# Optimization experiments

Measured on AMD Instinct MI355X. Metric: run time of the kernel, lower is better.

Reference implementation:

```python
import jax, jax.numpy as jnp
import numpy as np


def _safe_pow(v, p):
    # mimic torch.nan_to_num(pow(v, p), nan=0, posinf=0, neginf=0) for v >= 0
    out = jnp.where(v > 0, jnp.power(jnp.where(v > 0, v, 1.0), p), 0.0)
    return out.astype(jnp.float32)


def setup_inputs() -> dict:
    key = jax.random.key(0)
    k1, k2, k3 = jax.random.split(key, 3)
    N, E, Din, Dout = 20000, 4096, 128, 128
    x = jax.random.normal(k1, (N, Din), dtype=jnp.float32)
    H = jax.random.uniform(k2, (N, E), dtype=jnp.float32)
    W = jax.random.normal(k3, (Dout, Din), dtype=jnp.float32) * (1.0 / np.sqrt(Din))
    b = jnp.zeros((Dout,), dtype=jnp.float32)
    return {"x": x, "H": H, "W": W, "b": b}


def reference(x, H, W, b):
    # Dv^{-1/2}: node degrees; De^{-1}: hyperedge degrees.
    # torch.diag(...)**p with nan/inf->0 is exactly diagonal scaling, so we
    # use broadcasted vector scaling fused around the two GEMMs.
    dv = _safe_pow(jnp.sum(H, axis=-1), -0.5)   # [N]
    de = _safe_pow(jnp.sum(H, axis=0), -1.0)    # [E]
    x = dv[:, None] * x                          # Dv^{-1/2} x
    x = H.T @ x                                  # [E, Din]
    x = de[:, None] * x                          # De^{-1}
    x = H @ x                                    # [N, Din]
    x = dv[:, None] * x                          # Dv^{-1/2}
    return x @ W.T + b                           # Linear
```

## Files before the change

### kernel.cpp

```cpp
#include <hip/hip_runtime.h>
#include <hip/hip_bf16.h>
#include <stdint.h>


#define N_ 20000
#define E_ 4096
#define D_ 128
#define NPAD 20032
#define XTB_S 20032

typedef __attribute__((ext_vector_type(8))) short    bf16x8;
typedef __attribute__((ext_vector_type(4))) float    f32x4;
typedef __attribute__((ext_vector_type(8))) unsigned short us8;
typedef __attribute__((ext_vector_type(4))) unsigned short us4;

__device__ __forceinline__ unsigned short f2bf(float f) {
  unsigned u = __float_as_uint(f);
  u += 0x7FFFu + ((u >> 16) & 1u);
  return (unsigned short)(u >> 16);
}
__device__ __forceinline__ unsigned cvtpk(float lo, float hi) {
  unsigned r;
  asm("v_cvt_pk_bf16_f32 %0, %1, %2" : "=v"(r) : "v"(lo), "v"(hi));
  return r;
}
__device__ __forceinline__ void gload16(const unsigned short* g, unsigned short* l) {
  __builtin_amdgcn_global_load_lds(
      (const __attribute__((address_space(1))) unsigned int*)g,
      (__attribute__((address_space(3))) unsigned int*)l, 16, 0, 0);
}

__global__ __launch_bounds__(256) void k_pre(const float* __restrict__ H,
                                             const float* __restrict__ x,
                                             float* __restrict__ dv,
                                             unsigned short* __restrict__ Hb,
                                             unsigned short* __restrict__ xTb) {
  const int t = threadIdx.x, lane = t & 63, w = t >> 6;
  const int b = blockIdx.x;
  if (b >= 2500) {
    const size_t base = (size_t)(20000 + (b - 2500) * 8) * E_;
    for (int i = t; i < 4096; i += 256)
      *(us8*)&Hb[base + (size_t)i * 8] = (us8){0,0,0,0,0,0,0,0};
    if (b == 2500 && t < 128) {
#pragma unroll
      for (int c = 0; c < 4; ++c)
        *(us8*)&xTb[(size_t)t * XTB_S + 20000 + c * 8] = (us8){0,0,0,0,0,0,0,0};
    }
    return;
  }
  __shared__ float red[32];
  __shared__ float xt[8 * 128];
  const int n0 = b * 8;
  { int r = t >> 5, d4 = (t & 31) * 4;
    *(f32x4*)&xt[r * 128 + d4] = *(const f32x4*)(x + (size_t)(n0 + r) * D_ + d4); }
  float rs[8];
#pragma unroll
  for (int r = 0; r < 8; ++r) {
    rs[r] = 0.f;
    const float* rp = H + (size_t)(n0 + r) * E_;
    unsigned short* hp = Hb + (size_t)(n0 + r) * E_;
#pragma unroll
    for (int j = 0; j < 4; ++j) {
      f32x4 v = *(const f32x4*)(rp + j * 1024 + t * 4);
      rs[r] += (v.x + v.y) + (v.z + v.w);
      union { us4 v4; unsigned u32[2]; } un;
      un.u32[0] = cvtpk(v.x, v.y);
      un.u32[1] = cvtpk(v.z, v.w);
      *(us4*)(hp + j * 1024 + t * 4) = un.v4;
    }
  }
#pragma unroll
  for (int r = 0; r < 8; ++r)
#pragma unroll
    for (int off = 32; off; off >>= 1) rs[r] += __shfl_xor(rs[r], off);
  if (lane == 0) {
#pragma unroll
    for (int r = 0; r < 8; ++r) red[w * 8 + r] = rs[r];
  }
  __syncthreads();
  if (t < 8) {
    float s = red[t] + red[8 + t] + red[16 + t] + red[24 + t];
    float d = s > 0.f ? rsqrtf(s) : 0.f;
    dv[n0 + t] = d;
    red[t] = d;
  }
  __syncthreads();
  if (t < 128) {
    int d = t;
    float v[8];
#pragma unroll
    for (int r = 0; r < 8; ++r) v[r] = xt[r * 128 + d] * red[r];
    union { us8 v8; unsigned u32[4]; } un;
#pragma unroll
    for (int j = 0; j < 4; ++j) un.u32[j] = cvtpk(v[2 * j], v[2 * j + 1]);
    *(us8*)(xTb + (size_t)d * XTB_S + n0) = un.v8;
  }
}

__global__ __launch_bounds__(256) void k_fin(const float* __restrict__ desum,
                                             float* __restrict__ de) {
  int e = blockIdx.x * 256 + threadIdx.x;
  float s = desum[e];
  de[e] = s > 0.f ? 1.f / s : 0.f;
}

__global__ __launch_bounds__(256) void k_wb(const float* __restrict__ W,
                                            unsigned short* __restrict__ Wb) {
  int tid = blockIdx.x * 256 + threadIdx.x;
  float4 v = *(const float4*)(W + (size_t)tid * 4);
  union { us4 v; unsigned short u[4]; } un;
  un.u[0] = f2bf(v.x); un.u[1] = f2bf(v.y); un.u[2] = f2bf(v.z); un.u[3] = f2bf(v.w);
  *(us4*)(Wb + (size_t)tid * 4) = un.v;
}

__global__ __launch_bounds__(256) void k_gemm1(const unsigned short* __restrict__ Hb,
                                               const unsigned short* __restrict__ xTb,
                                               float* __restrict__ partialT,
                                               float* __restrict__ desum) {
  __shared__ unsigned short lH[2][64 * 64];
  __shared__ unsigned short lX[2][128 * 64];
  const int t = threadIdx.x, lane = t & 63, w = t >> 6;
  const int eb = blockIdx.x & 63, s = blockIdx.x >> 6;
  const int e0 = eb * 64;
  const int nsteps = 39 + (s == 7);
  const int g0 = s * 39;
  const int lrow = lane >> 3, lslot = lane & 7;
  const int bswz = (lslot ^ lrow) << 3;
  const int wy = w >> 1, wx = w & 1;
  const int ep = t & 31, q = t >> 5;
  const int er0 = 2 * ep, er1 = 2 * ep + 1;
  const int sl0 = (q ^ (er0 & 7)) << 3, sl1 = (q ^ (er1 & 7)) << 3;

  f32x4 acc[4][2];
  f32x4 accC[2];
#pragma unroll
  for (int i = 0; i < 4; ++i)
#pragma unroll
    for (int j = 0; j < 2; ++j) acc[i][j] = (f32x4){0.f, 0.f, 0.f, 0.f};
  accC[0] = (f32x4){0.f, 0.f, 0.f, 0.f};
  accC[1] = (f32x4){0.f, 0.f, 0.f, 0.f};
  bf16x8 ones;
#pragma unroll
  for (int i = 0; i < 8; ++i) ones[i] = (short)0x3F80;

  unsigned hr[8];
  auto LOADH = [&](int g) {
    const unsigned short* p = Hb + (size_t)(g * 64 + q * 8) * E_ + e0 + er0;
#pragma unroll
    for (int j = 0; j < 8; ++j) hr[j] = *(const unsigned*)(p + (size_t)j * E_);
  };
  auto WRITEH = [&](int bufi) {
    union { bf16x8 v; unsigned u[4]; } lo, hi;
#pragma unroll
    for (int p = 0; p < 4; ++p) {
      lo.u[p] = (hr[2 * p] & 0xFFFFu) | (hr[2 * p + 1] << 16);
      hi.u[p] = (hr[2 * p] >> 16) | (hr[2 * p + 1] & 0xFFFF0000u);
    }
    *(bf16x8*)&lH[bufi][er0 * 64 + sl0] = lo.v;
    *(bf16x8*)&lH[bufi][er1 * 64 + sl1] = hi.v;
  };
  auto GLOADX = [&](int g, int bufi) {
#pragma unroll
    for (int i = 0; i < 4; ++i) {
      int c = w * 4 + i;
      gload16(xTb + (size_t)(8 * c + lrow) * XTB_S + g * 64 + bswz,
              &lX[bufi][c * 512]);
    }
  };

  LOADH(g0); GLOADX(g0, 0); WRITEH(0);
  __syncthreads();
  int cur = 0;
  for (int it = 0; it < nsteps; ++it) {
    bool hn = it + 1 < nsteps;
    if (hn) { LOADH(g0 + it + 1); GLOADX(g0 + it + 1, cur ^ 1); }
    const int kg = lane >> 4, fr = lane & 15;
    bf16x8 ax[4][2], bh[2][2];
#pragma unroll
    for (int mi = 0; mi < 4; ++mi) {
      int m = wy * 64 + mi * 16 + fr;
#pragma unroll
      for (int kk = 0; kk < 2; ++kk)
        ax[mi][kk] = *(const bf16x8*)&lX[cur][m * 64 + (((kk * 4 + kg) ^ (m & 7)) << 3)];
    }
#pragma unroll
    for (int ni = 0; ni < 2; ++ni) {
      int n = wx * 32 + ni * 16 + fr;
#pragma unroll
      for (int kk = 0; kk < 2; ++kk)
        bh[ni][kk] = *(const bf16x8*)&lH[cur][n * 64 + (((kk * 4 + kg) ^ (n & 7)) << 3)];
    }
#pragma unroll
    for (int kk = 0; kk < 2; ++kk)
#pragma unroll
      for (int mi = 0; mi < 4; ++mi)
#pragma unroll
        for (int ni = 0; ni < 2; ++ni)
          acc[mi][ni] = __builtin_amdgcn_mfma_f32_16x16x32_bf16(ax[mi][kk], bh[ni][kk], acc[mi][ni], 0, 0, 0);
    if (wy == 0) {
#pragma unroll
      for (int kk = 0; kk < 2; ++kk)
#pragma unroll
        for (int ni = 0; ni < 2; ++ni)
          accC[ni] = __builtin_amdgcn_mfma_f32_16x16x32_bf16(ones, bh[ni][kk], accC[ni], 0, 0, 0);
    }
    if (hn) WRITEH(cur ^ 1);
    __syncthreads();
    cur ^= 1;
  }
  const int kg = lane >> 4, fr = lane & 15;
  if (wy == 0 && kg == 0) {
#pragma unroll
    for (int ni = 0; ni < 2; ++ni)
      atomicAdd(&desum[e0 + wx * 32 + ni * 16 + fr], accC[ni][0]);
  }
#pragma unroll
  for (int mi = 0; mi < 4; ++mi)
#pragma unroll
    for (int ni = 0; ni < 2; ++ni)
#pragma unroll
      for (int r = 0; r < 4; ++r) {
        int d = wy * 64 + mi * 16 + kg * 4 + r;
        int e = e0 + wx * 32 + ni * 16 + fr;
        partialT[((size_t)s * 128 + d) * E_ + e] = acc[mi][ni][r];
      }
}

__global__ __launch_bounds__(256) void k_reduce1(const float* __restrict__ partialT,
                                                 const float* __restrict__ de,
                                                 unsigned short* __restrict__ x3T) {
  int tid = blockIdx.x * 256 + threadIdx.x;
  int d = tid >> 12, e = tid & 4095;
  float s = 0.f;
#pragma unroll
  for (int ss = 0; ss < 8; ++ss) s += partialT[((size_t)ss * 128 + d) * E_ + e];
  x3T[(size_t)d * E_ + e] = f2bf(de[e] * s);
}

__global__ __launch_bounds__(256) void k_gemm2(const unsigned short* __restrict__ Hb,
                                               const unsigned short* __restrict__ x3T,
                                               const unsigned short* __restrict__ Wb,
                                               const float* __restrict__ dv,
                                               const float* __restrict__ bias,
                                               float* __restrict__ out) {
  __shared__ unsigned short sm[2 * 64 * 64 + 2 * 128 * 64];
  __shared__ unsigned short lW[128 * 128];
  unsigned short (*lA)[64 * 64]  = (unsigned short (*)[64 * 64])sm;
  unsigned short (*lB)[128 * 64] = (unsigned short (*)[128 * 64])(sm + 2 * 64 * 64);
  unsigned short* lC = sm;
  const int t = threadIdx.x, lane = t & 63, w = t >> 6;
  const int n0b = blockIdx.x * 64;
  const int lrow = lane >> 3, lslot = lane & 7;
  const int bswz = (lslot ^ lrow) << 3;
  const int wy = w >> 1, wx = w & 1;

  {
    int j = t >> 1;
#pragma unroll
    for (int jj = 0; jj < 4; ++jj) {
      int dofs = (t & 1) * 64 + jj * 16;
      const us8* src = (const us8*)(Wb + (size_t)j * 128 + dofs);
      *(us8*)&lW[j * 128 + dofs]     = src[0];
      *(us8*)&lW[j * 128 + dofs + 8] = src[1];
    }
  }

  auto GLOADA = [&](int g, int bufi) {
#pragma unroll
    for (int i = 0; i < 2; ++i) {
      int c = w * 2 + i;
      gload16(Hb + (size_t)(n0b + 8 * c + lrow) * E_ + g * 64 + bswz,
              &lA[bufi][c * 512]);
    }
  };
  auto GLOADB = [&](int g, int bufi) {
#pragma unroll
    for (int i = 0; i < 4; ++i) {
      int c = w * 4 + i;
      gload16(x3T + (size_t)(8 * c + lrow) * E_ + g * 64 + bswz,
              &lB[bufi][c * 512]);
    }
  };

  f32x4 acc[2][4];
#pragma unroll
  for (int i = 0; i < 2; ++i)
#pragma unroll
    for (int j = 0; j < 4; ++j) acc[i][j] = (f32x4){0.f, 0.f, 0.f, 0.f};

  GLOADA(0, 0); GLOADB(0, 0);
  __syncthreads();
  int cur = 0;
  for (int it = 0; it < 64; ++it) {
    bool hn = it < 63;
    if (hn) { GLOADA(it + 1, cur ^ 1); GLOADB(it + 1, cur ^ 1); }
    const int kg = lane >> 4, fr = lane & 15;
    bf16x8 af[2][2], bfr[4][2];
#pragma unroll
    for (int mi = 0; mi < 2; ++mi) {
      int m = wy * 32 + mi * 16 + fr;
#pragma unroll
      for (int kk = 0; kk < 2; ++kk)
        af[mi][kk] = *(const bf16x8*)&lA[cur][m * 64 + (((kk * 4 + kg) ^ (m & 7)) << 3)];
    }
#pragma unroll
    for (int ni = 0; ni < 4; ++ni) {
      int d = wx * 64 + ni * 16 + fr;
#pragma unroll
      for (int kk = 0; kk < 2; ++kk)
        bfr[ni][kk] = *(const bf16x8*)&lB[cur][d * 64 + (((kk * 4 + kg) ^ (d & 7)) << 3)];
    }
#pragma unroll
    for (int kk = 0; kk < 2; ++kk)
#pragma unroll
      for (int mi = 0; mi < 2; ++mi)
#pragma unroll
        for (int ni = 0; ni < 4; ++ni)
          acc[mi][ni] = __builtin_amdgcn_mfma_f32_16x16x32_bf16(af[mi][kk], bfr[ni][kk], acc[mi][ni], 0, 0, 0);
    __syncthreads();
    cur ^= 1;
  }
#pragma unroll
  for (int mi = 0; mi < 2; ++mi) {
    float dvv[4];
#pragma unroll
    for (int r = 0; r < 4; ++r)
      dvv[r] = dv[min(n0b + wy * 32 + mi * 16 + (lane >> 4) * 4 + r, N_ - 1)];
#pragma unroll
    for (int ni = 0; ni < 4; ++ni)
#pragma unroll
      for (int r = 0; r < 4; ++r) {
        int row = wy * 32 + mi * 16 + (lane >> 4) * 4 + r;
        int col = wx * 64 + ni * 16 + (lane & 15);
        lC[row * 136 + col] = f2bf(acc[mi][ni][r] * dvv[r]);
      }
  }
  __syncthreads();
  f32x4 acc2[2][4];
#pragma unroll
  for (int i = 0; i < 2; ++i)
#pragma unroll
    for (int j = 0; j < 4; ++j) acc2[i][j] = (f32x4){0.f, 0.f, 0.f, 0.f};
#pragma unroll
  for (int ks = 0; ks < 4; ++ks) {
    int kofs = ks * 32 + (lane >> 4) * 8;
    bf16x8 a2[2], b2[4];
#pragma unroll
    for (int mi = 0; mi < 2; ++mi) {
      int m = wy * 32 + mi * 16 + (lane & 15);
      a2[mi] = *(const bf16x8*)&lC[m * 136 + kofs];
    }
#pragma unroll
    for (int ni = 0; ni < 4; ++ni) {
      int j = wx * 64 + ni * 16 + (lane & 15);
      b2[ni] = *(const bf16x8*)&lW[j * 128 + kofs];
    }
#pragma unroll
    for (int mi = 0; mi < 2; ++mi)
#pragma unroll
      for (int ni = 0; ni < 4; ++ni)
        acc2[mi][ni] = __builtin_amdgcn_mfma_f32_16x16x32_bf16(a2[mi], b2[ni], acc2[mi][ni], 0, 0, 0);
  }
#pragma unroll
  for (int mi = 0; mi < 2; ++mi)
#pragma unroll
    for (int ni = 0; ni < 4; ++ni) {
      int j = wx * 64 + ni * 16 + (lane & 15);
      float bb = bias[j];
#pragma unroll
      for (int r = 0; r < 4; ++r) {
        int n = n0b + wy * 32 + mi * 16 + (lane >> 4) * 4 + r;
        if (n < N_) out[(size_t)n * D_ + j] = acc2[mi][ni][r] + bb;
      }
    }
}

extern "C" void kernel_launch(void* const* d_in, const int* in_sizes, int n_in,
                              void* d_out, int out_size, void* d_ws, size_t ws_size,
                              hipStream_t stream) {
  const float* x = (const float*)d_in[0];
  const float* H = (const float*)d_in[1];
  const float* W = (const float*)d_in[2];
  const float* b = (const float*)d_in[3];
  float* out = (float*)d_out;
  char* ws = (char*)d_ws;
  float*          desum    = (float*)(ws);
  float*          de       = (float*)(ws + 16384);
  float*          dv       = (float*)(ws + 32768);
  unsigned short* Wb       = (unsigned short*)(ws + 112896);
  unsigned short* xTb      = (unsigned short*)(ws + 145664);
  unsigned short* x3T      = (unsigned short*)(ws + 5273856);
  float*          partialT = (float*)(ws + 6322432);
  unsigned short* Hb       = (unsigned short*)(ws + 23099648);

  hipMemsetAsync(desum, 0, 16384, stream);
  k_pre<<<2504, 256, 0, stream>>>(H, x, dv, Hb, xTb);
  k_wb<<<16, 256, 0, stream>>>(W, Wb);
  k_gemm1<<<512, 256, 0, stream>>>(Hb, xTb, partialT, desum);
  k_fin<<<16, 256, 0, stream>>>(desum, de);
  k_reduce1<<<2048, 256, 0, stream>>>(partialT, de, x3T);
  k_gemm2<<<313, 256, 0, stream>>>(Hb, x3T, Wb, dv, b, out);
}
```

Baseline: 240.7 us.

## Fold degree finalize and W conversion into neighbors; halve gemm2 row tile

Replaces the desum atomics and memset with per-split partial edge-degree stores, which k_reduce1 sums and inverts inline. k_reduce1 is vectorized to 8 elements per thread. The standalone W-to-bf16 kernel is removed and W is converted inside k_gemm2, which now uses 32-row tiles across 625 blocks for better CU coverage. This removes three launches and a memset, at the cost of redundant W conversion in every gemm2 block and less reuse of x3T per block.

```diff
diff --git a/kernel.cpp b/kernel.cpp
--- a/kernel.cpp
+++ b/kernel.cpp
@@ -6,7 +6,6 @@
 #define N_ 20000
 #define E_ 4096
 #define D_ 128
-#define NPAD 20032
 #define XTB_S 20032
 
 typedef __attribute__((ext_vector_type(8))) short    bf16x8;
@@ -97,26 +96,10 @@
   }
 }
 
-__global__ __launch_bounds__(256) void k_fin(const float* __restrict__ desum,
-                                             float* __restrict__ de) {
-  int e = blockIdx.x * 256 + threadIdx.x;
-  float s = desum[e];
-  de[e] = s > 0.f ? 1.f / s : 0.f;
-}
-
-__global__ __launch_bounds__(256) void k_wb(const float* __restrict__ W,
-                                            unsigned short* __restrict__ Wb) {
-  int tid = blockIdx.x * 256 + threadIdx.x;
-  float4 v = *(const float4*)(W + (size_t)tid * 4);
-  union { us4 v; unsigned short u[4]; } un;
-  un.u[0] = f2bf(v.x); un.u[1] = f2bf(v.y); un.u[2] = f2bf(v.z); un.u[3] = f2bf(v.w);
-  *(us4*)(Wb + (size_t)tid * 4) = un.v;
-}
-
 __global__ __launch_bounds__(256) void k_gemm1(const unsigned short* __restrict__ Hb,
                                                const unsigned short* __restrict__ xTb,
                                                float* __restrict__ partialT,
-                                               float* __restrict__ desum) {
+                                               float* __restrict__ desumP) {
   __shared__ unsigned short lH[2][64 * 64];
   __shared__ unsigned short lX[2][128 * 64];
   const int t = threadIdx.x, lane = t & 63, w = t >> 6;
@@ -212,7 +195,7 @@
   if (wy == 0 && kg == 0) {
 #pragma unroll
     for (int ni = 0; ni < 2; ++ni)
-      atomicAdd(&desum[e0 + wx * 32 + ni * 16 + fr], accC[ni][0]);
+      desumP[s * E_ + e0 + wx * 32 + ni * 16 + fr] = accC[ni][0];
   }
 #pragma unroll
   for (int mi = 0; mi < 4; ++mi)
@@ -227,51 +210,73 @@
 }
 
 __global__ __launch_bounds__(256) void k_reduce1(const float* __restrict__ partialT,
-                                                 const float* __restrict__ de,
+                                                 const float* __restrict__ desumP,
                                                  unsigned short* __restrict__ x3T) {
   int tid = blockIdx.x * 256 + threadIdx.x;
-  int d = tid >> 12, e = tid & 4095;
-  float s = 0.f;
-#pragma unroll
-  for (int ss = 0; ss < 8; ++ss) s += partialT[((size_t)ss * 128 + d) * E_ + e];
-  x3T[(size_t)d * E_ + e] = f2bf(de[e] * s);
+  int d = tid >> 9;
+  int e0 = (tid & 511) * 8;
+  f32x4 sA = {0.f,0.f,0.f,0.f}, sB = {0.f,0.f,0.f,0.f};
+  f32x4 dA = {0.f,0.f,0.f,0.f}, dB = {0.f,0.f,0.f,0.f};
+#pragma unroll
+  for (int ss = 0; ss < 8; ++ss) {
+    const float* p = partialT + ((size_t)ss * 128 + d) * E_ + e0;
+    sA += *(const f32x4*)p;
+    sB += *(const f32x4*)(p + 4);
+    const float* qd = desumP + ss * E_ + e0;
+    dA += *(const f32x4*)qd;
+    dB += *(const f32x4*)(qd + 4);
+  }
+  float sv[8] = {sA.x, sA.y, sA.z, sA.w, sB.x, sB.y, sB.z, sB.w};
+  float dvv[8] = {dA.x, dA.y, dA.z, dA.w, dB.x, dB.y, dB.z, dB.w};
+  float o[8];
+#pragma unroll
+  for (int i = 0; i < 8; ++i)
+    o[i] = dvv[i] > 0.f ? sv[i] / dvv[i] : 0.f;
+  union { us8 v8; unsigned u32[4]; } un;
+#pragma unroll
+  for (int j = 0; j < 4; ++j) un.u32[j] = cvtpk(o[2 * j], o[2 * j + 1]);
+  *(us8*)(x3T + (size_t)d * E_ + e0) = un.v8;
 }
 
 __global__ __launch_bounds__(256) void k_gemm2(const unsigned short* __restrict__ Hb,
                                                const unsigned short* __restrict__ x3T,
-                                               const unsigned short* __restrict__ Wb,
+                                               const float* __restrict__ W,
                                                const float* __restrict__ dv,
                                                const float* __restrict__ bias,
                                                float* __restrict__ out) {
-  __shared__ unsigned short sm[2 * 64 * 64 + 2 * 128 * 64];
-  __shared__ unsigned short lW[128 * 128];
-  unsigned short (*lA)[64 * 64]  = (unsigned short (*)[64 * 64])sm;
-  unsigned short (*lB)[128 * 64] = (unsigned short (*)[128 * 64])(sm + 2 * 64 * 64);
+  __shared__ unsigned short sm[2 * 32 * 64 + 2 * 128 * 64];
+  __shared__ unsigned short lW[128 * 136];
+  unsigned short (*lA)[32 * 64]  = (unsigned short (*)[32 * 64])sm;
+  unsigned short (*lB)[128 * 64] = (unsigned short (*)[128 * 64])(sm + 2 * 32 * 64);
   unsigned short* lC = sm;
   const int t = threadIdx.x, lane = t & 63, w = t >> 6;
-  const int n0b = blockIdx.x * 64;
+  const int n0b = blockIdx.x * 32;
   const int lrow = lane >> 3, lslot = lane & 7;
   const int bswz = (lslot ^ lrow) << 3;
   const int wy = w >> 1, wx = w & 1;
 
   {
     int j = t >> 1;
+    int dbase = (t & 1) * 64;
 #pragma unroll
     for (int jj = 0; jj < 4; ++jj) {
-      int dofs = (t & 1) * 64 + jj * 16;
-      const us8* src = (const us8*)(Wb + (size_t)j * 128 + dofs);
-      *(us8*)&lW[j * 128 + dofs]     = src[0];
-      *(us8*)&lW[j * 128 + dofs + 8] = src[1];
+      int dofs = dbase + jj * 16;
+      const float* wp = W + (size_t)j * 128 + dofs;
+      f32x4 a = *(const f32x4*)wp,       bq = *(const f32x4*)(wp + 4);
+      f32x4 c = *(const f32x4*)(wp + 8), dq = *(const f32x4*)(wp + 12);
+      union { us8 v; unsigned u[4]; } u0, u1;
+      u0.u[0] = cvtpk(a.x, a.y);  u0.u[1] = cvtpk(a.z, a.w);
+      u0.u[2] = cvtpk(bq.x, bq.y); u0.u[3] = cvtpk(bq.z, bq.w);
+      u1.u[0] = cvtpk(c.x, c.y);  u1.u[1] = cvtpk(c.z, c.w);
+      u1.u[2] = cvtpk(dq.x, dq.y); u1.u[3] = cvtpk(dq.z, dq.w);
+      *(us8*)&lW[j * 136 + dofs]     = u0.v;
+      *(us8*)&lW[j * 136 + dofs + 8] = u1.v;
     }
   }
 
   auto GLOADA = [&](int g, int bufi) {
-#pragma unroll
-    for (int i = 0; i < 2; ++i) {
-      int c = w * 2 + i;
-      gload16(Hb + (size_t)(n0b + 8 * c + lrow) * E_ + g * 64 + bswz,
-              &lA[bufi][c * 512]);
-    }
+    gload16(Hb + (size_t)(n0b + 8 * w + lrow) * E_ + g * 64 + bswz,
+            &lA[bufi][w * 512]);
   };
   auto GLOADB = [&](int g, int bufi) {
 #pragma unroll
@@ -282,11 +287,9 @@
     }
   };
 
-  f32x4 acc[2][4];
-#pragma unroll
-  for (int i = 0; i < 2; ++i)
-#pragma unroll
-    for (int j = 0; j < 4; ++j) acc[i][j] = (f32x4){0.f, 0.f, 0.f, 0.f};
+  f32x4 acc[4];
+#pragma unroll
+  for (int j = 0; j < 4; ++j) acc[j] = (f32x4){0.f, 0.f, 0.f, 0.f};
 
   GLOADA(0, 0); GLOADB(0, 0);
   __syncthreads();
@@ -295,14 +298,11 @@
     bool hn = it < 63;
     if (hn) { GLOADA(it + 1, cur ^ 1); GLOADB(it + 1, cur ^ 1); }
     const int kg = lane >> 4, fr = lane & 15;
-    bf16x8 af[2][2], bfr[4][2];
-#pragma unroll
-    for (int mi = 0; mi < 2; ++mi) {
-      int m = wy * 32 + mi * 16 + fr;
-#pragma unroll
-      for (int kk = 0; kk < 2; ++kk)
-        af[mi][kk] = *(const bf16x8*)&lA[cur][m * 64 + (((kk * 4 + kg) ^ (m & 7)) << 3)];
-    }
+    const int m = wy * 16 + fr;
+    bf16x8 af[2], bfr[4][2];
+#pragma unroll
+    for (int kk = 0; kk < 2; ++kk)
+      af[kk] = *(const bf16x8*)&lA[cur][m * 64 + (((kk * 4 + kg) ^ (m & 7)) << 3)];
 #pragma unroll
     for (int ni = 0; ni < 4; ++ni) {
       int d = wx * 64 + ni * 16 + fr;
@@ -313,66 +313,49 @@
 #pragma unroll
     for (int kk = 0; kk < 2; ++kk)
 #pragma unroll
-      for (int mi = 0; mi < 2; ++mi)
-#pragma unroll
-        for (int ni = 0; ni < 4; ++ni)
-          acc[mi][ni] = __builtin_amdgcn_mfma_f32_16x16x32_bf16(af[mi][kk], bfr[ni][kk], acc[mi][ni], 0, 0, 0);
+      for (int ni = 0; ni < 4; ++ni)
+        acc[ni] = __builtin_amdgcn_mfma_f32_16x16x32_bf16(af[kk], bfr[ni][kk], acc[ni], 0, 0, 0);
     __syncthreads();
     cur ^= 1;
   }
-#pragma unroll
-  for (int mi = 0; mi < 2; ++mi) {
-    float dvv[4];
-#pragma unroll
-    for (int r = 0; r < 4; ++r)
-      dvv[r] = dv[min(n0b + wy * 32 + mi * 16 + (lane >> 4) * 4 + r, N_ - 1)];
+  const int kg = lane >> 4, fr = lane & 15;
+  float dvv[4];
+#pragma unroll
+  for (int r = 0; r < 4; ++r) dvv[r] = dv[n0b + wy * 16 + kg * 4 + r];
+#pragma unroll
+  for (int ni = 0; ni < 4; ++ni)
+#pragma unroll
+    for (int r = 0; r < 4; ++r) {
+      int row = wy * 16 + kg * 4 + r;
+      int col = wx * 64 + ni * 16 + fr;
+      lC[row * 136 + col] = f2bf(acc[ni][r] * dvv[r]);
+    }
+  __syncthreads();
+  f32x4 acc2[4];
+#pragma unroll
+  for (int j = 0; j < 4; ++j) acc2[j] = (f32x4){0.f, 0.f, 0.f, 0.f};
+#pragma unroll
+  for (int ks = 0; ks < 4; ++ks) {
+    int kofs = ks * 32 + kg * 8;
+    bf16x8 a2 = *(const bf16x8*)&lC[(wy * 16 + fr) * 136 + kofs];
+    bf16x8 b2[4];
 #pragma unroll
     for (int ni = 0; ni < 4; ++ni)
-#pragma unroll
-      for (int r = 0; r < 4; ++r) {
-        int row = wy * 32 + mi * 16 + (lane >> 4) * 4 + r;
-        int col = wx * 64 + ni * 16 + (lane & 15);
-        lC[row * 136 + col] = f2bf(acc[mi][ni][r] * dvv[r]);
-      }
-  }
-  __syncthreads();
-  f32x4 acc2[2][4];
-#pragma unroll
-  for (int i = 0; i < 2; ++i)
-#pragma unroll
-    for (int j = 0; j < 4; ++j) acc2[i][j] = (f32x4){0.f, 0.f, 0.f, 0.f};
-#pragma unroll
-  for (int ks = 0; ks < 4; ++ks) {
-    int kofs = ks * 32 + (lane >> 4) * 8;
-    bf16x8 a2[2], b2[4];
-#pragma unroll
-    for (int mi = 0; mi < 2; ++mi) {
-      int m = wy * 32 + mi * 16 + (lane & 15);
-      a2[mi] = *(const bf16x8*)&lC[m * 136 + kofs];
-    }
-#pragma unroll
-    for (int ni = 0; ni < 4; ++ni) {
-      int j = wx * 64 + ni * 16 + (lane & 15);
-      b2[ni] = *(const bf16x8*)&lW[j * 128 + kofs];
-    }
-#pragma unroll
-    for (int mi = 0; mi < 2; ++mi)
-#pragma unroll
-      for (int ni = 0; ni < 4; ++ni)
-        acc2[mi][ni] = __builtin_amdgcn_mfma_f32_16x16x32_bf16(a2[mi], b2[ni], acc2[mi][ni], 0, 0, 0);
-  }
-#pragma unroll
-  for (int mi = 0; mi < 2; ++mi)
-#pragma unroll
-    for (int ni = 0; ni < 4; ++ni) {
-      int j = wx * 64 + ni * 16 + (lane & 15);
-      float bb = bias[j];
-#pragma unroll
-      for (int r = 0; r < 4; ++r) {
-        int n = n0b + wy * 32 + mi * 16 + (lane >> 4) * 4 + r;
-        if (n < N_) out[(size_t)n * D_ + j] = acc2[mi][ni][r] + bb;
-      }
-    }
+      b2[ni] = *(const bf16x8*)&lW[(wx * 64 + ni * 16 + fr) * 136 + kofs];
+#pragma unroll
+    for (int ni = 0; ni < 4; ++ni)
+      acc2[ni] = __builtin_amdgcn_mfma_f32_16x16x32_bf16(a2, b2[ni], acc2[ni], 0, 0, 0);
+  }
+#pragma unroll
+  for (int ni = 0; ni < 4; ++ni) {
+    int j = wx * 64 + ni * 16 + fr;
+    float bb = bias[j];
+#pragma unroll
+    for (int r = 0; r < 4; ++r) {
+      int n = n0b + wy * 16 + kg * 4 + r;
+      out[(size_t)n * D_ + j] = acc2[ni][r] + bb;
+    }
+  }
 }
 
 extern "C" void kernel_launch(void* const* d_in, const int* in_sizes, int n_in,
@@ -384,20 +367,15 @@
   const float* b = (const float*)d_in[3];
   float* out = (float*)d_out;
   char* ws = (char*)d_ws;
-  float*          desum    = (float*)(ws);
-  float*          de       = (float*)(ws + 16384);
-  float*          dv       = (float*)(ws + 32768);
-  unsigned short* Wb       = (unsigned short*)(ws + 112896);
-  unsigned short* xTb      = (unsigned short*)(ws + 145664);
-  unsigned short* x3T      = (unsigned short*)(ws + 5273856);
-  float*          partialT = (float*)(ws + 6322432);
-  unsigned short* Hb       = (unsigned short*)(ws + 23099648);
-
-  hipMemsetAsync(desum, 0, 16384, stream);
+  float*          desumP   = (float*)(ws);
+  float*          dv       = (float*)(ws + 131072);
+  unsigned short* xTb      = (unsigned short*)(ws + 211200);
+  unsigned short* x3T      = (unsigned short*)(ws + 5339392);
+  float*          partialT = (float*)(ws + 6387968);
+  unsigned short* Hb       = (unsigned short*)(ws + 23165184);
+
   k_pre<<<2504, 256, 0, stream>>>(H, x, dv, Hb, xTb);
-  k_wb<<<16, 256, 0, stream>>>(W, Wb);
-  k_gemm1<<<512, 256, 0, stream>>>(Hb, xTb, partialT, desum);
-  k_fin<<<16, 256, 0, stream>>>(desum, de);
-  k_reduce1<<<2048, 256, 0, stream>>>(partialT, de, x3T);
-  k_gemm2<<<313, 256, 0, stream>>>(Hb, x3T, Wb, dv, b, out);
-}
+  k_gemm1<<<512, 256, 0, stream>>>(Hb, xTb, partialT, desumP);
+  k_reduce1<<<256, 256, 0, stream>>>(partialT, desumP, x3T);
+  k_gemm2<<<625, 256, 0, stream>>>(Hb, x3T, W, dv, b, out);
+}
```

New measurement: 269.0 us. 1.12x slower.

## Widen GEMM1 edge tiles, split K sixteen ways, fuse degree finalize and W conversion

Applied to the files above, without the earlier changes.

GEMM1 now uses 128-wide hyperedge tiles and a 16-way split of the node dimension, so more work shares each x tile load. Per-split edge-degree partials replace the atomics and memset, and the reduce kernel sums them with vectorized loads, doing the reciprocal scaling in place. The separate k_fin and k_wb launches are removed, and W is converted to bf16 inside GEMM2 with a swizzled LDS layout. The price is twice the partialT traffic written and reduced, a larger LDS footprint, and more accumulator registers under launch_bounds(256,2).

```diff
diff --git a/kernel.cpp b/kernel.cpp
--- a/kernel.cpp
+++ b/kernel.cpp
@@ -6,8 +6,8 @@
 #define N_ 20000
 #define E_ 4096
 #define D_ 128
-#define NPAD 20032
 #define XTB_S 20032
+#define SPLIT 16
 
 typedef __attribute__((ext_vector_type(8))) short    bf16x8;
 typedef __attribute__((ext_vector_type(4))) float    f32x4;
@@ -97,67 +97,56 @@
   }
 }
 
-__global__ __launch_bounds__(256) void k_fin(const float* __restrict__ desum,
-                                             float* __restrict__ de) {
-  int e = blockIdx.x * 256 + threadIdx.x;
-  float s = desum[e];
-  de[e] = s > 0.f ? 1.f / s : 0.f;
-}
-
-__global__ __launch_bounds__(256) void k_wb(const float* __restrict__ W,
-                                            unsigned short* __restrict__ Wb) {
-  int tid = blockIdx.x * 256 + threadIdx.x;
-  float4 v = *(const float4*)(W + (size_t)tid * 4);
-  union { us4 v; unsigned short u[4]; } un;
-  un.u[0] = f2bf(v.x); un.u[1] = f2bf(v.y); un.u[2] = f2bf(v.z); un.u[3] = f2bf(v.w);
-  *(us4*)(Wb + (size_t)tid * 4) = un.v;
-}
-
-__global__ __launch_bounds__(256) void k_gemm1(const unsigned short* __restrict__ Hb,
-                                               const unsigned short* __restrict__ xTb,
-                                               float* __restrict__ partialT,
-                                               float* __restrict__ desum) {
-  __shared__ unsigned short lH[2][64 * 64];
+__global__ __launch_bounds__(256, 2) void k_gemm1(const unsigned short* __restrict__ Hb,
+                                                  const unsigned short* __restrict__ xTb,
+                                                  float* __restrict__ partialT,
+                                                  float* __restrict__ desumP) {
+  __shared__ unsigned short lH[2][128 * 68];
   __shared__ unsigned short lX[2][128 * 64];
   const int t = threadIdx.x, lane = t & 63, w = t >> 6;
-  const int eb = blockIdx.x & 63, s = blockIdx.x >> 6;
-  const int e0 = eb * 64;
-  const int nsteps = 39 + (s == 7);
-  const int g0 = s * 39;
+  const int bid = blockIdx.x;
+  const int j0 = bid >> 3;
+  const int s  = (bid & 7) * 2 + (j0 >> 5);
+  const int eb = j0 & 31;
+  const int e0 = eb * 128;
+  const int g0 = (s * 313) >> 4;
+  const int g1 = ((s + 1) * 313) >> 4;
   const int lrow = lane >> 3, lslot = lane & 7;
   const int bswz = (lslot ^ lrow) << 3;
   const int wy = w >> 1, wx = w & 1;
-  const int ep = t & 31, q = t >> 5;
-  const int er0 = 2 * ep, er1 = 2 * ep + 1;
-  const int sl0 = (q ^ (er0 & 7)) << 3, sl1 = (q ^ (er1 & 7)) << 3;
-
-  f32x4 acc[4][2];
+
+  f32x4 acc[4][4];
   f32x4 accC[2];
 #pragma unroll
   for (int i = 0; i < 4; ++i)
 #pragma unroll
-    for (int j = 0; j < 2; ++j) acc[i][j] = (f32x4){0.f, 0.f, 0.f, 0.f};
+    for (int j = 0; j < 4; ++j) acc[i][j] = (f32x4){0.f, 0.f, 0.f, 0.f};
   accC[0] = (f32x4){0.f, 0.f, 0.f, 0.f};
   accC[1] = (f32x4){0.f, 0.f, 0.f, 0.f};
   bf16x8 ones;
 #pragma unroll
   for (int i = 0; i < 8; ++i) ones[i] = (short)0x3F80;
 
-  unsigned hr[8];
+  unsigned hr[16];
   auto LOADH = [&](int g) {
-    const unsigned short* p = Hb + (size_t)(g * 64 + q * 8) * E_ + e0 + er0;
-#pragma unroll
-    for (int j = 0; j < 8; ++j) hr[j] = *(const unsigned*)(p + (size_t)j * E_);
+    const unsigned short* p = Hb + (size_t)(g * 64 + w * 16) * E_ + e0 + 2 * lane;
+#pragma unroll
+    for (int j = 0; j < 16; ++j)
+      hr[j] = *(const unsigned*)(p + (size_t)j * E_);
   };
   auto WRITEH = [&](int bufi) {
-    union { bf16x8 v; unsigned u[4]; } lo, hi;
-#pragma unroll
-    for (int p = 0; p < 4; ++p) {
-      lo.u[p] = (hr[2 * p] & 0xFFFFu) | (hr[2 * p + 1] << 16);
-      hi.u[p] = (hr[2 * p] >> 16) | (hr[2 * p + 1] & 0xFFFF0000u);
-    }
-    *(bf16x8*)&lH[bufi][er0 * 64 + sl0] = lo.v;
-    *(bf16x8*)&lH[bufi][er1 * 64 + sl1] = hi.v;
+#pragma unroll
+    for (int j = 0; j < 2; ++j) {
+      union { bf16x8 v; unsigned u[4]; } lo, hi;
+#pragma unroll
+      for (int p2 = 0; p2 < 4; ++p2) {
+        unsigned a = hr[j * 8 + 2 * p2], b = hr[j * 8 + 2 * p2 + 1];
+        lo.u[p2] = (a & 0xFFFFu) | (b << 16);
+        hi.u[p2] = (a >> 16) | (b & 0xFFFF0000u);
+      }
+      *(bf16x8*)&lH[bufi][(2 * lane) * 68 + (2 * w + j) * 8]     = lo.v;
+      *(bf16x8*)&lH[bufi][(2 * lane + 1) * 68 + (2 * w + j) * 8] = hi.v;
+    }
   };
   auto GLOADX = [&](int g, int bufi) {
 #pragma unroll
@@ -171,11 +160,11 @@
   LOADH(g0); GLOADX(g0, 0); WRITEH(0);
   __syncthreads();
   int cur = 0;
-  for (int it = 0; it < nsteps; ++it) {
-    bool hn = it + 1 < nsteps;
-    if (hn) { LOADH(g0 + it + 1); GLOADX(g0 + it + 1, cur ^ 1); }
+  for (int it = g0; it < g1; ++it) {
+    bool hn = it + 1 < g1;
+    if (hn) { LOADH(it + 1); GLOADX(it + 1, cur ^ 1); }
     const int kg = lane >> 4, fr = lane & 15;
-    bf16x8 ax[4][2], bh[2][2];
+    bf16x8 ax[4][2], bh[4][2];
 #pragma unroll
     for (int mi = 0; mi < 4; ++mi) {
       int m = wy * 64 + mi * 16 + fr;
@@ -184,62 +173,78 @@
         ax[mi][kk] = *(const bf16x8*)&lX[cur][m * 64 + (((kk * 4 + kg) ^ (m & 7)) << 3)];
     }
 #pragma unroll
-    for (int ni = 0; ni < 2; ++ni) {
-      int n = wx * 32 + ni * 16 + fr;
+    for (int ni = 0; ni < 4; ++ni) {
+      int n = wx * 64 + ni * 16 + fr;
 #pragma unroll
       for (int kk = 0; kk < 2; ++kk)
-        bh[ni][kk] = *(const bf16x8*)&lH[cur][n * 64 + (((kk * 4 + kg) ^ (n & 7)) << 3)];
+        bh[ni][kk] = *(const bf16x8*)&lH[cur][n * 68 + (kk * 4 + kg) * 8];
     }
 #pragma unroll
     for (int kk = 0; kk < 2; ++kk)
 #pragma unroll
       for (int mi = 0; mi < 4; ++mi)
 #pragma unroll
-        for (int ni = 0; ni < 2; ++ni)
+        for (int ni = 0; ni < 4; ++ni)
           acc[mi][ni] = __builtin_amdgcn_mfma_f32_16x16x32_bf16(ax[mi][kk], bh[ni][kk], acc[mi][ni], 0, 0, 0);
-    if (wy == 0) {
-#pragma unroll
-      for (int kk = 0; kk < 2; ++kk)
-#pragma unroll
-        for (int ni = 0; ni < 2; ++ni)
-          accC[ni] = __builtin_amdgcn_mfma_f32_16x16x32_bf16(ones, bh[ni][kk], accC[ni], 0, 0, 0);
-    }
+#pragma unroll
+    for (int kk = 0; kk < 2; ++kk)
+#pragma unroll
+      for (int ci = 0; ci < 2; ++ci)
+        accC[ci] = __builtin_amdgcn_mfma_f32_16x16x32_bf16(ones, bh[wy * 2 + ci][kk], accC[ci], 0, 0, 0);
     if (hn) WRITEH(cur ^ 1);
     __syncthreads();
     cur ^= 1;
   }
   const int kg = lane >> 4, fr = lane & 15;
-  if (wy == 0 && kg == 0) {
-#pragma unroll
-    for (int ni = 0; ni < 2; ++ni)
-      atomicAdd(&desum[e0 + wx * 32 + ni * 16 + fr], accC[ni][0]);
+  if (kg == 0) {
+#pragma unroll
+    for (int ci = 0; ci < 2; ++ci)
+      desumP[s * E_ + e0 + wx * 64 + (wy * 2 + ci) * 16 + fr] = accC[ci][0];
   }
 #pragma unroll
   for (int mi = 0; mi < 4; ++mi)
 #pragma unroll
-    for (int ni = 0; ni < 2; ++ni)
+    for (int ni = 0; ni < 4; ++ni)
 #pragma unroll
       for (int r = 0; r < 4; ++r) {
         int d = wy * 64 + mi * 16 + kg * 4 + r;
-        int e = e0 + wx * 32 + ni * 16 + fr;
+        int e = e0 + wx * 64 + ni * 16 + fr;
         partialT[((size_t)s * 128 + d) * E_ + e] = acc[mi][ni][r];
       }
 }
 
 __global__ __launch_bounds__(256) void k_reduce1(const float* __restrict__ partialT,
-                                                 const float* __restrict__ de,
+                                                 const float* __restrict__ desumP,
                                                  unsigned short* __restrict__ x3T) {
   int tid = blockIdx.x * 256 + threadIdx.x;
-  int d = tid >> 12, e = tid & 4095;
-  float s = 0.f;
-#pragma unroll
-  for (int ss = 0; ss < 8; ++ss) s += partialT[((size_t)ss * 128 + d) * E_ + e];
-  x3T[(size_t)d * E_ + e] = f2bf(de[e] * s);
+  int d = tid >> 9;
+  int e0 = (tid & 511) * 8;
+  f32x4 sA = {0.f,0.f,0.f,0.f}, sB = {0.f,0.f,0.f,0.f};
+  f32x4 dA = {0.f,0.f,0.f,0.f}, dB = {0.f,0.f,0.f,0.f};
+#pragma unroll
+  for (int ss = 0; ss < SPLIT; ++ss) {
+    const float* p = partialT + ((size_t)ss * 128 + d) * E_ + e0;
+    sA += *(const f32x4*)p;
+    sB += *(const f32x4*)(p + 4);
+    const float* qd = desumP + ss * E_ + e0;
+    dA += *(const f32x4*)qd;
+    dB += *(const f32x4*)(qd + 4);
+  }
+  float sv[8] = {sA.x, sA.y, sA.z, sA.w, sB.x, sB.y, sB.z, sB.w};
+  float dvv[8] = {dA.x, dA.y, dA.z, dA.w, dB.x, dB.y, dB.z, dB.w};
+  float o[8];
+#pragma unroll
+  for (int i = 0; i < 8; ++i)
+    o[i] = dvv[i] > 0.f ? sv[i] / dvv[i] : 0.f;
+  union { us8 v8; unsigned u32[4]; } un;
+#pragma unroll
+  for (int j = 0; j < 4; ++j) un.u32[j] = cvtpk(o[2 * j], o[2 * j + 1]);
+  *(us8*)(x3T + (size_t)d * E_ + e0) = un.v8;
 }
 
 __global__ __launch_bounds__(256) void k_gemm2(const unsigned short* __restrict__ Hb,
                                                const unsigned short* __restrict__ x3T,
-                                               const unsigned short* __restrict__ Wb,
+                                               const float* __restrict__ W,
                                                const float* __restrict__ dv,
                                                const float* __restrict__ bias,
                                                float* __restrict__ out) {
@@ -256,12 +261,20 @@
 
   {
     int j = t >> 1;
+    int sb = (t & 1) * 8;
 #pragma unroll
     for (int jj = 0; jj < 4; ++jj) {
-      int dofs = (t & 1) * 64 + jj * 16;
-      const us8* src = (const us8*)(Wb + (size_t)j * 128 + dofs);
-      *(us8*)&lW[j * 128 + dofs]     = src[0];
-      *(us8*)&lW[j * 128 + dofs + 8] = src[1];
+      int s0 = sb + jj * 2;
+      const float* wp = W + (size_t)j * 128 + s0 * 8;
+      f32x4 a = *(const f32x4*)wp,       b4 = *(const f32x4*)(wp + 4);
+      f32x4 c = *(const f32x4*)(wp + 8), d4 = *(const f32x4*)(wp + 12);
+      union { us8 v; unsigned u[4]; } u0, u1;
+      u0.u[0] = cvtpk(a.x, a.y);   u0.u[1] = cvtpk(a.z, a.w);
+      u0.u[2] = cvtpk(b4.x, b4.y); u0.u[3] = cvtpk(b4.z, b4.w);
+      u1.u[0] = cvtpk(c.x, c.y);   u1.u[1] = cvtpk(c.z, c.w);
+      u1.u[2] = cvtpk(d4.x, d4.y); u1.u[3] = cvtpk(d4.z, d4.w);
+      *(us8*)&lW[j * 128 + ((s0 ^ (j & 7)) << 3)]       = u0.v;
+      *(us8*)&lW[j * 128 + (((s0 + 1) ^ (j & 7)) << 3)] = u1.v;
     }
   }
 
@@ -343,17 +356,18 @@
     for (int j = 0; j < 4; ++j) acc2[i][j] = (f32x4){0.f, 0.f, 0.f, 0.f};
 #pragma unroll
   for (int ks = 0; ks < 4; ++ks) {
-    int kofs = ks * 32 + (lane >> 4) * 8;
+    const int kg = lane >> 4, fr = lane & 15;
+    int kofs = ks * 32 + kg * 8;
     bf16x8 a2[2], b2[4];
 #pragma unroll
     for (int mi = 0; mi < 2; ++mi) {
-      int m = wy * 32 + mi * 16 + (lane & 15);
+      int m = wy * 32 + mi * 16 + fr;
       a2[mi] = *(const bf16x8*)&lC[m * 136 + kofs];
     }
 #pragma unroll
     for (int ni = 0; ni < 4; ++ni) {
-      int j = wx * 64 + ni * 16 + (lane & 15);
-      b2[ni] = *(const bf16x8*)&lW[j * 128 + kofs];
+      int j2 = wx * 64 + ni * 16 + fr;
+      b2[ni] = *(const bf16x8*)&lW[j2 * 128 + (((ks * 4 + kg) ^ (j2 & 7)) << 3)];
     }
 #pragma unroll
     for (int mi = 0; mi < 2; ++mi)
@@ -365,12 +379,12 @@
   for (int mi = 0; mi < 2; ++mi)
 #pragma unroll
     for (int ni = 0; ni < 4; ++ni) {
-      int j = wx * 64 + ni * 16 + (lane & 15);
-      float bb = bias[j];
+      int j2 = wx * 64 + ni * 16 + (lane & 15);
+      float bb = bias[j2];
 #pragma unroll
       for (int r = 0; r < 4; ++r) {
         int n = n0b + wy * 32 + mi * 16 + (lane >> 4) * 4 + r;
-        if (n < N_) out[(size_t)n * D_ + j] = acc2[mi][ni][r] + bb;
+        if (n < N_) out[(size_t)n * D_ + j2] = acc2[mi][ni][r] + bb;
       }
     }
 }
@@ -384,20 +398,15 @@
   const float* b = (const float*)d_in[3];
   float* out = (float*)d_out;
   char* ws = (char*)d_ws;
-  float*          desum    = (float*)(ws);
-  float*          de       = (float*)(ws + 16384);
-  float*          dv       = (float*)(ws + 32768);
-  unsigned short* Wb       = (unsigned short*)(ws + 112896);
-  unsigned short* xTb      = (unsigned short*)(ws + 145664);
-  unsigned short* x3T      = (unsigned short*)(ws + 5273856);
-  float*          partialT = (float*)(ws + 6322432);
-  unsigned short* Hb       = (unsigned short*)(ws + 23099648);
-
-  hipMemsetAsync(desum, 0, 16384, stream);
+  float*          desumP   = (float*)(ws);
+  float*          dv       = (float*)(ws + 262144);
+  unsigned short* xTb      = (unsigned short*)(ws + 342272);
+  unsigned short* x3T      = (unsigned short*)(ws + 5470464);
+  float*          partialT = (float*)(ws + 6519040);
+  unsigned short* Hb       = (unsigned short*)(ws + 40073472);
+
   k_pre<<<2504, 256, 0, stream>>>(H, x, dv, Hb, xTb);
-  k_wb<<<16, 256, 0, stream>>>(W, Wb);
-  k_gemm1<<<512, 256, 0, stream>>>(Hb, xTb, partialT, desum);
-  k_fin<<<16, 256, 0, stream>>>(desum, de);
-  k_reduce1<<<2048, 256, 0, stream>>>(partialT, de, x3T);
-  k_gemm2<<<313, 256, 0, stream>>>(Hb, x3T, Wb, dv, b, out);
-}
+  k_gemm1<<<512, 256, 0, stream>>>(Hb, xTb, partialT, desumP);
+  k_reduce1<<<256, 256, 0, stream>>>(partialT, desumP, x3T);
+  k_gemm2<<<313, 256, 0, stream>>>(Hb, x3T, W, dv, b, out);
+}
```

After: 480.4 us. 2x slower.
